# Optimization experiments

Measured on AMD Instinct MI355X. Metric: run time of the kernel, lower is better.

## Reference

```python
import jax, jax.numpy as jnp
import numpy as np

B, H, T, D = 2, 16, 2048, 64


def setup_inputs() -> dict:
    key = jax.random.key(0)
    kq, kk, kv, km = jax.random.split(key, 4)
    q = jax.random.normal(kq, (B, H, T, D), dtype=jnp.float32)
    k = jax.random.normal(kk, (B, H, T, D), dtype=jnp.float32)
    v = jax.random.normal(kv, (B, H, T, D), dtype=jnp.float32)
    # boolean mask, True = masked out (broadcast over batch and heads)
    mask = jax.random.randint(km, (1, 1, T, T), 0, 2).astype(jnp.bool_)
    return {"q": q, "k": k, "v": v, "mask": mask}


def reference(q, k, v, mask):
    scale = q.shape[-1] ** (-0.5)
    # [B,H,T,T] score matrix (materialized, as in the original)
    scores = jnp.einsum("bhqd,bhkd->bhqk", q, k) * scale
    scores = jnp.where(mask, jnp.float32(-10000.0), scores)
    attn = jax.nn.softmax(scores, axis=-1)
    attn = jnp.where(mask, jnp.float32(0.0), attn)
    return jnp.einsum("bhqk,bhkd->bhqd", attn, v)
```

## Files before the change

### kernel.cpp

```cpp
#include <hip/hip_runtime.h>
#include <hip/hip_bf16.h>

typedef __bf16 bf16x8 __attribute__((ext_vector_type(8)));
typedef __bf16 bf16x4 __attribute__((ext_vector_type(4)));
typedef float  f32x4  __attribute__((ext_vector_type(4)));

#define T_SEQ 2048
#define D_HEAD 64
#define BH_N 32
#define NT_TILES (T_SEQ / 64)
#define IMG_BYTES 16384
#define SCALE_LOG2 0.18033688011112042f

#define WS_IMG ((size_t)0)
#define WS_MB  ((size_t)16u << 20)

static __device__ __forceinline__ f32x4 mfma32(bf16x8 a, bf16x8 b, f32x4 c) {
    return __builtin_amdgcn_mfma_f32_16x16x32_bf16(a, b, c, 0, 0, 0);
}

static __device__ __forceinline__ float fast_exp2(float x) {
#if __has_builtin(__builtin_amdgcn_exp2f)
    return __builtin_amdgcn_exp2f(x);
#else
    return exp2f(x);
#endif
}

static __device__ __forceinline__ void gload16(const void* g, void* l, int lane) {
#if __has_builtin(__builtin_amdgcn_global_load_lds)
    (void)lane;
    __builtin_amdgcn_global_load_lds(
        (const __attribute__((address_space(1))) void*)g,
        (__attribute__((address_space(3))) void*)l, 16, 0, 0);
#else
    *((f32x4*)l + lane) = *(const f32x4*)g;
#endif
}


__global__ __launch_bounds__(256) void prep_kv(const float* __restrict__ k,
                                               const float* __restrict__ v,
                                               char* __restrict__ img) {
    __shared__ __bf16 t[64][72];
    const int bh = blockIdx.y, tt = blockIdx.x, tid = threadIdx.x;
    char* ob = img + ((size_t)bh * NT_TILES + tt) * IMG_BYTES;
    {
        const int kr = tid >> 2, qd = tid & 3, ke = kr & 7;
        const size_t base = ((size_t)bh * T_SEQ + tt * 64 + kr) * D_HEAD + qd * 16;
        const float4 a0 = *(const float4*)(k + base);
        const float4 a1 = *(const float4*)(k + base + 4);
        const float4 a2 = *(const float4*)(k + base + 8);
        const float4 a3 = *(const float4*)(k + base + 12);
        bf16x8 w0, w1;
        w0[0]=(__bf16)a0.x; w0[1]=(__bf16)a0.y; w0[2]=(__bf16)a0.z; w0[3]=(__bf16)a0.w;
        w0[4]=(__bf16)a1.x; w0[5]=(__bf16)a1.y; w0[6]=(__bf16)a1.z; w0[7]=(__bf16)a1.w;
        w1[0]=(__bf16)a2.x; w1[1]=(__bf16)a2.y; w1[2]=(__bf16)a2.z; w1[3]=(__bf16)a2.w;
        w1[4]=(__bf16)a3.x; w1[5]=(__bf16)a3.y; w1[6]=(__bf16)a3.z; w1[7]=(__bf16)a3.w;
        *(bf16x8*)(ob + kr * 128 + (((2 * qd + 0) ^ ke) << 4)) = w0;
        *(bf16x8*)(ob + kr * 128 + (((2 * qd + 1) ^ ke) << 4)) = w1;
    }
    {
        const int tr = tid >> 4, c4 = (tid & 15) * 4;
        const float* src = v + ((size_t)bh * T_SEQ + tt * 64) * D_HEAD;
#pragma unroll
        for (int p = 0; p < 4; ++p) {
            const int row = p * 16 + tr;
            const float4 f = *(const float4*)(src + row * D_HEAD + c4);
            t[c4+0][row] = (__bf16)f.x; t[c4+1][row] = (__bf16)f.y;
            t[c4+2][row] = (__bf16)f.z; t[c4+3][row] = (__bf16)f.w;
        }
        __syncthreads();
        const int d = tid >> 2;
        char* vb = ob + 8192 + d * 128;
#pragma unroll
        for (int mi = 0; mi < 2; ++mi) {
            const int m  = (tid & 3) * 2 + mi;
            const int u  = m ^ (d & 7);
            const int k0 = (u & 1) * 32 + (u >> 1) * 4;
            const bf16x4 lo = *(const bf16x4*)&t[d][k0];
            const bf16x4 hi = *(const bf16x4*)&t[d][k0 + 16];
            *(bf16x8*)(vb + m * 16) = __builtin_shufflevector(lo, hi, 0,1,2,3,4,5,6,7);
        }
    }
}

__global__ void mpack(const int* __restrict__ m, unsigned long long* __restrict__ mb) {
    const int i = blockIdx.x * 256 + threadIdx.x;
    const unsigned long long b = __ballot(m[i] != 0);
    if ((threadIdx.x & 63) == 0) mb[i >> 6] = b;
}


__global__ __launch_bounds__(256, 4) void attn9(
    const float* __restrict__ q, const char* __restrict__ img,
    const unsigned long long* __restrict__ mb, float* __restrict__ out)
{
    const int qt = blockIdx.x;
    const int bh = blockIdx.y;
    const int tid = threadIdx.x, wave = tid >> 6, lane = tid & 63;
    const int g = lane >> 4, ln = lane & 15;
    const int qp = wave & 1, kh = wave >> 1;

    __shared__ __align__(16) char smem[33280];
    float* Ep = (float*)smem;
    float* Os = (float*)(smem + 32768);

    const int qw = qt * 64 + qp * 32;

    bf16x8 qf[2][2];
#pragma unroll
    for (int qs = 0; qs < 2; ++qs) {
        const float* qpt = q + ((size_t)bh * T_SEQ + qw + qs * 16 + ln) * D_HEAD + g * 8;
#pragma unroll
        for (int kc = 0; kc < 2; ++kc) {
            const float4 f0 = *(const float4*)(qpt + kc * 32);
            const float4 f1 = *(const float4*)(qpt + kc * 32 + 4);
            qf[qs][kc][0]=(__bf16)(f0.x*SCALE_LOG2); qf[qs][kc][1]=(__bf16)(f0.y*SCALE_LOG2);
            qf[qs][kc][2]=(__bf16)(f0.z*SCALE_LOG2); qf[qs][kc][3]=(__bf16)(f0.w*SCALE_LOG2);
            qf[qs][kc][4]=(__bf16)(f1.x*SCALE_LOG2); qf[qs][kc][5]=(__bf16)(f1.y*SCALE_LOG2);
            qf[qs][kc][6]=(__bf16)(f1.z*SCALE_LOG2); qf[qs][kc][7]=(__bf16)(f1.w*SCALE_LOG2);
        }
    }

    f32x4 o[2][4];
#pragma unroll
    for (int qs = 0; qs < 2; ++qs)
#pragma unroll
        for (int mt = 0; mt < 4; ++mt) o[qs][mt] = (f32x4){0.f, 0.f, 0.f, 0.f};
    f32x4 osum[2] = { (f32x4){0.f,0.f,0.f,0.f}, (f32x4){0.f,0.f,0.f,0.f} };
    const bf16x8 ones8 = { (__bf16)1.0f, (__bf16)1.0f, (__bf16)1.0f, (__bf16)1.0f,
                           (__bf16)1.0f, (__bf16)1.0f, (__bf16)1.0f, (__bf16)1.0f };

    const char* ibase = img + (size_t)bh * (NT_TILES * (size_t)IMG_BYTES);
    const unsigned long long* mrow0 = mb + (size_t)(qw + ln) * 32;
    const unsigned long long* mrow1 = mb + (size_t)(qw + 16 + ln) * 32;

    {
        const char* src = ibase + wave * 4096 + lane * 16;
        char* dst = smem + wave * 4096;
#pragma unroll
        for (int i = 0; i < 4; ++i) gload16(src + i * 1024, dst + i * 1024, lane);
    }
    unsigned long long mw0 = mrow0[0], mw1 = mrow1[0];
    __syncthreads();

    for (int kt = 0; kt < NT_TILES; ++kt) {
        const int b = kt & 1;
        unsigned long long mn0 = 0, mn1 = 0;
        if (kt < NT_TILES - 1) {
            const char* src = ibase + (size_t)(kt + 1) * IMG_BYTES + wave * 4096 + lane * 16;
            char* dst = smem + (b ^ 1) * 16384 + wave * 4096;
#pragma unroll
            for (int i = 0; i < 4; ++i) gload16(src + i * 1024, dst + i * 1024, lane);
            mn0 = mrow0[kt + 1]; mn1 = mrow1[kt + 1];
        }

        const char* KB = smem + b * 16384;
        const char* VB = KB + 8192;

        const unsigned nbs0 = (~(unsigned)(mw0 >> (kh << 5))) >> (g * 4);
        const unsigned nbs1 = (~(unsigned)(mw1 >> (kh << 5))) >> (g * 4);

        bf16x8 pa8[2];
#pragma unroll
        for (int ntl = 0; ntl < 2; ++ntl) {
            const int row = (2 * kh + ntl) * 16 + ln;
            const int rb = row * 128 + ((g ^ (ln & 7)) << 4);
            const bf16x8 a0 = *(const bf16x8*)(KB + rb);
            const bf16x8 a1 = *(const bf16x8*)(KB + (rb ^ 64));
#pragma unroll
            for (int qs = 0; qs < 2; ++qs) {
                f32x4 c = (f32x4){0.f, 0.f, 0.f, 0.f};
                c = mfma32(a0, qf[qs][0], c);
                c = mfma32(a1, qf[qs][1], c);
                const unsigned nbs = qs ? nbs1 : nbs0;
#pragma unroll
                for (int r = 0; r < 4; ++r) {
                    const float e = fast_exp2(c[r]);
                    const int keep = (int)(nbs << (31 - (ntl * 16 + r))) >> 31;
                    const float p = __builtin_bit_cast(float,
                        __builtin_bit_cast(unsigned, e) & (unsigned)keep);
                    pa8[qs][ntl * 4 + r] = (__bf16)p;
                }
            }
        }

#pragma unroll
        for (int qs = 0; qs < 2; ++qs) osum[qs] = mfma32(pa8[qs], ones8, osum[qs]);
#pragma unroll
        for (int mt = 0; mt < 4; ++mt) {
            const bf16x8 vv = *(const bf16x8*)(VB + (mt * 16 + ln) * 128
                                + ((((g << 1) | kh) ^ (ln & 7)) << 4));
#pragma unroll
            for (int qs = 0; qs < 2; ++qs)
                o[qs][mt] = mfma32(pa8[qs], vv, o[qs][mt]);
        }

        __syncthreads();
        mw0 = mn0; mw1 = mn1;
    }

#pragma unroll
    for (int qs = 0; qs < 2; ++qs) {
#pragma unroll
        for (int mt = 0; mt < 4; ++mt)
#pragma unroll
            for (int r = 0; r < 4; ++r)
                Ep[(size_t)kh * 4096 + (qp * 32 + qs * 16 + g * 4 + r) * 64 + mt * 16 + ln] = o[qs][mt][r];
        if (ln == 0) {
#pragma unroll
            for (int r = 0; r < 4; ++r)
                Os[kh * 64 + qp * 32 + qs * 16 + g * 4 + r] = osum[qs][r];
        }
    }
    __syncthreads();
#pragma unroll
    for (int p = 0; p < 4; ++p) {
        const int idx = p * 256 + tid;
        const int row = idx >> 4, c4 = (idx & 15) * 4;
        const float l = Os[row] + Os[64 + row];
        const float inv = (l > 0.f) ? (1.f / l) : 0.f;
        const float4 a  = *(const float4*)(Ep + row * 64 + c4);
        const float4 b4 = *(const float4*)(Ep + 4096 + row * 64 + c4);
        const float4 st = { (a.x + b4.x) * inv, (a.y + b4.y) * inv,
                            (a.z + b4.z) * inv, (a.w + b4.w) * inv };
        *(float4*)(out + ((size_t)bh * T_SEQ + qt * 64 + row) * D_HEAD + c4) = st;
    }
}

extern "C" void kernel_launch(void* const* d_in, const int* in_sizes, int n_in,
                              void* d_out, int out_size, void* d_ws, size_t ws_size,
                              hipStream_t stream) {
    const float* q    = (const float*)d_in[0];
    const float* k    = (const float*)d_in[1];
    const float* v    = (const float*)d_in[2];
    const int*   mask = (const int*)d_in[3];
    float*       out  = (float*)d_out;

    char* img = (char*)d_ws + WS_IMG;
    unsigned long long* mbw = (unsigned long long*)((char*)d_ws + WS_MB);

    prep_kv<<<dim3(NT_TILES, BH_N), 256, 0, stream>>>(k, v, img);
    mpack<<<(T_SEQ * T_SEQ) / 256, 256, 0, stream>>>(mask, mbw);
    attn9<<<dim3(NT_TILES, BH_N), 256, 0, stream>>>(q, img, mbw, out);
}
```

Baseline: 161.3 us.

## Double query tile per block to 128 rows with 8 waves sharing K/V tiles

Each workgroup now processes 128 query rows using 512 threads (4 query pairs by 2 key halves), so every K/V tile staged into shared memory serves twice as many queries and global K/V traffic is halved. Blocks are launched on a 1-D grid with a swizzled mapping that interleaves batch-heads, intended to improve L2 locality across concurrently running blocks. The epilogue reduction runs in two passes to fit the existing shared buffer. This halves the grid size, which may reduce occupancy, and adds a sync in the epilogue.

```diff
diff --git a/kernel.cpp b/kernel.cpp
--- a/kernel.cpp
+++ b/kernel.cpp
@@ -9,6 +9,7 @@
 #define D_HEAD 64
 #define BH_N 32
 #define NT_TILES (T_SEQ / 64)
+#define QT_N 16
 #define IMG_BYTES 16384
 #define SCALE_LOG2 0.18033688011112042f
 
@@ -92,21 +93,24 @@
 }
 
 
-__global__ __launch_bounds__(256, 4) void attn9(
+__global__ __launch_bounds__(512, 4) void attn10(
     const float* __restrict__ q, const char* __restrict__ img,
     const unsigned long long* __restrict__ mb, float* __restrict__ out)
 {
-    const int qt = blockIdx.x;
-    const int bh = blockIdx.y;
+    const int l   = blockIdx.x;
+    const int m_  = l >> 3;
+    const int bh  = ((l & 7) << 2) | (m_ & 3);
+    const int qt  = m_ >> 2;
+
     const int tid = threadIdx.x, wave = tid >> 6, lane = tid & 63;
     const int g = lane >> 4, ln = lane & 15;
-    const int qp = wave & 1, kh = wave >> 1;
+    const int qp = wave & 3, kh = wave >> 2;
 
     __shared__ __align__(16) char smem[33280];
     float* Ep = (float*)smem;
     float* Os = (float*)(smem + 32768);
 
-    const int qw = qt * 64 + qp * 32;
+    const int qw = qt * 128 + qp * 32;
 
     bf16x8 qf[2][2];
 #pragma unroll
@@ -137,10 +141,10 @@
     const unsigned long long* mrow1 = mb + (size_t)(qw + 16 + ln) * 32;
 
     {
-        const char* src = ibase + wave * 4096 + lane * 16;
-        char* dst = smem + wave * 4096;
-#pragma unroll
-        for (int i = 0; i < 4; ++i) gload16(src + i * 1024, dst + i * 1024, lane);
+        const char* src = ibase + wave * 2048 + lane * 16;
+        char* dst = smem + wave * 2048;
+#pragma unroll
+        for (int i = 0; i < 2; ++i) gload16(src + i * 1024, dst + i * 1024, lane);
     }
     unsigned long long mw0 = mrow0[0], mw1 = mrow1[0];
     __syncthreads();
@@ -149,10 +153,10 @@
         const int b = kt & 1;
         unsigned long long mn0 = 0, mn1 = 0;
         if (kt < NT_TILES - 1) {
-            const char* src = ibase + (size_t)(kt + 1) * IMG_BYTES + wave * 4096 + lane * 16;
-            char* dst = smem + (b ^ 1) * 16384 + wave * 4096;
-#pragma unroll
-            for (int i = 0; i < 4; ++i) gload16(src + i * 1024, dst + i * 1024, lane);
+            const char* src = ibase + (size_t)(kt + 1) * IMG_BYTES + wave * 2048 + lane * 16;
+            char* dst = smem + (b ^ 1) * 16384 + wave * 2048;
+#pragma unroll
+            for (int i = 0; i < 2; ++i) gload16(src + i * 1024, dst + i * 1024, lane);
             mn0 = mrow0[kt + 1]; mn1 = mrow1[kt + 1];
         }
 
@@ -202,30 +206,37 @@
     }
 
 #pragma unroll
-    for (int qs = 0; qs < 2; ++qs) {
-#pragma unroll
-        for (int mt = 0; mt < 4; ++mt)
-#pragma unroll
-            for (int r = 0; r < 4; ++r)
-                Ep[(size_t)kh * 4096 + (qp * 32 + qs * 16 + g * 4 + r) * 64 + mt * 16 + ln] = o[qs][mt][r];
-        if (ln == 0) {
-#pragma unroll
-            for (int r = 0; r < 4; ++r)
-                Os[kh * 64 + qp * 32 + qs * 16 + g * 4 + r] = osum[qs][r];
-        }
-    }
-    __syncthreads();
-#pragma unroll
-    for (int p = 0; p < 4; ++p) {
-        const int idx = p * 256 + tid;
-        const int row = idx >> 4, c4 = (idx & 15) * 4;
-        const float l = Os[row] + Os[64 + row];
-        const float inv = (l > 0.f) ? (1.f / l) : 0.f;
-        const float4 a  = *(const float4*)(Ep + row * 64 + c4);
-        const float4 b4 = *(const float4*)(Ep + 4096 + row * 64 + c4);
-        const float4 st = { (a.x + b4.x) * inv, (a.y + b4.y) * inv,
-                            (a.z + b4.z) * inv, (a.w + b4.w) * inv };
-        *(float4*)(out + ((size_t)bh * T_SEQ + qt * 64 + row) * D_HEAD + c4) = st;
+    for (int pass = 0; pass < 2; ++pass) {
+        if ((qp >> 1) == pass) {
+            const int qpl = qp & 1;
+#pragma unroll
+            for (int qs = 0; qs < 2; ++qs) {
+#pragma unroll
+                for (int mt = 0; mt < 4; ++mt)
+#pragma unroll
+                    for (int r = 0; r < 4; ++r)
+                        Ep[(size_t)kh * 4096 + (qpl * 32 + qs * 16 + g * 4 + r) * 64 + mt * 16 + ln] = o[qs][mt][r];
+                if (ln == 0) {
+#pragma unroll
+                    for (int r = 0; r < 4; ++r)
+                        Os[kh * 64 + qpl * 32 + qs * 16 + g * 4 + r] = osum[qs][r];
+                }
+            }
+        }
+        __syncthreads();
+#pragma unroll
+        for (int p2 = 0; p2 < 2; ++p2) {
+            const int idx = p2 * 512 + tid;
+            const int row = idx >> 4, c4 = (idx & 15) * 4;
+            const float sl = Os[row] + Os[64 + row];
+            const float inv = (sl > 0.f) ? (1.f / sl) : 0.f;
+            const float4 a  = *(const float4*)(Ep + row * 64 + c4);
+            const float4 b4 = *(const float4*)(Ep + 4096 + row * 64 + c4);
+            const float4 st = { (a.x + b4.x) * inv, (a.y + b4.y) * inv,
+                                (a.z + b4.z) * inv, (a.w + b4.w) * inv };
+            *(float4*)(out + ((size_t)bh * T_SEQ + qt * 128 + pass * 64 + row) * D_HEAD + c4) = st;
+        }
+        if (pass == 0) __syncthreads();
     }
 }
 
@@ -243,5 +254,5 @@
 
     prep_kv<<<dim3(NT_TILES, BH_N), 256, 0, stream>>>(k, v, img);
     mpack<<<(T_SEQ * T_SEQ) / 256, 256, 0, stream>>>(mask, mbw);
-    attn9<<<dim3(NT_TILES, BH_N), 256, 0, stream>>>(q, img, mbw, out);
-}
+    attn10<<<dim3(QT_N * BH_N), 512, 0, stream>>>(q, img, mbw, out);
+}
```

Result: no change. 162.7 us (+0.9%).
